# Kernel optimization log

Measured on AMD Instinct MI355X. Metric: run time of the kernel, lower is better.

## Reference

```python
import jax, jax.numpy as jnp
import numpy as np

B, N_LATENT, N_NUISANCE, N_OUT = 2048, 64, 16, 2048


def setup_inputs() -> dict:
    key = jax.random.key(0)
    ks = jax.random.split(key, 6)
    z = jax.random.normal(ks[0], (B, N_LATENT + N_NUISANCE), dtype=jnp.float32)
    size_factor = jax.random.uniform(ks[1], (B, 1), dtype=jnp.float32) + 0.5
    # nn.Linear(n_latent, n_out, bias=False): store as [L, O] for z0 @ W
    amat_w = jax.random.normal(ks[2], (N_LATENT, N_OUT), dtype=jnp.float32) / np.sqrt(N_LATENT).astype(np.float32)
    amat_site = jax.random.normal(ks[3], (N_NUISANCE, N_LATENT, N_OUT), dtype=jnp.float32)
    offsets = jax.random.normal(ks[4], (N_NUISANCE, N_OUT), dtype=jnp.float32)
    px_r = jax.random.normal(ks[5], (N_OUT,), dtype=jnp.float32)
    return {"z": z, "size_factor": size_factor, "amat_w": amat_w,
            "amat_site": amat_site, "offsets": offsets, "px_r": px_r}


def reference(z, size_factor, amat_w, amat_site, offsets, px_r):
    n_nuisance = offsets.shape[0]
    nuisance_oh = z[..., -n_nuisance:]          # [B, N] one-hot site indicator
    z0 = z[..., :-n_nuisance]                   # [B, L] latent part
    x1 = z0 @ amat_w                            # [B, O] shared linear decoder
    nuisance_ids = jnp.argmax(nuisance_oh, axis=-1)  # [B] int ids
    # dropout(p=0.1) in eval mode == identity; .detach() -> stop_gradient
    z0_d = jax.lax.stop_gradient(z0)
    As = amat_site[nuisance_ids]                # [B, L, O] per-sample gathered weights
    x2 = jnp.einsum('bl,blo->bo', z0_d, As)     # batched matvec reduction over L
    mu = jax.nn.softmax(x1 + x2 + offsets[nuisance_ids], axis=-1)  # [B, O]
    mu = mu * size_factor                       # scale by per-cell size factor
    theta = jnp.exp(px_r)                       # NB inverse-dispersion, [O]
    return mu, theta
```

## Files before the change

### kernel.cpp

```cpp
#include <hip/hip_runtime.h>
#include <hip/hip_bf16.h>

#define NB 2048
#define NL 64
#define NN 16
#define NROW 80
#define NO 2048
#define TPB 256
#define OPT 8
#define G 4
#define MAXWL (NB / G + NN)
#define MBLK (NN * NL * NO / 4 / TPB)

typedef unsigned int   u32;
typedef unsigned short u16;

__device__ __forceinline__ float bflo(u32 u) { union { u32 i; float f; } c; c.i = u << 16;          return c.f; }
__device__ __forceinline__ float bfhi(u32 u) { union { u32 i; float f; } c; c.i = u & 0xffff0000u;  return c.f; }
__device__ __forceinline__ u16 f2bf(float f) { __hip_bfloat16 h = __float2bfloat16(f); return *(u16*)&h; }

__global__ __launch_bounds__(TPB) void prep(
    const float* __restrict__ W,
    const float* __restrict__ A,
    const float* __restrict__ z,
    const float* __restrict__ pxr,
    u16* __restrict__ M,
    u32* __restrict__ counts,
    u32* __restrict__ perm,
    u32* __restrict__ wl,
    u32* __restrict__ nit,
    float* __restrict__ out)
{
    const int blk = blockIdx.x;
    const int tid = threadIdx.x;

    if (blk < MBLK) {
        size_t t    = (size_t)blk * TPB + tid;
        size_t base = t * 4;
        float4 w = *(const float4*)(W + (base & (size_t)(NL * NO - 1)));
        float4 a = *(const float4*)(A + base);
        ushort4 m;
        m.x = f2bf(w.x + a.x);
        m.y = f2bf(w.y + a.y);
        m.z = f2bf(w.z + a.z);
        m.w = f2bf(w.w + a.w);
        *(ushort4*)(M + base) = m;
        return;
    }

    if (blk == MBLK) {
        __shared__ u32 lc[NN];
        __shared__ u32 choff[NN + 1];
        if (tid < NN) lc[tid] = 0;
        __syncthreads();
        #pragma unroll
        for (int k = 0; k < NB / TPB; ++k) {
            const int b = k * TPB + tid;
            const float* zp = z + (size_t)b * NROW + NL;
            float4 v0 = *(const float4*)(zp);
            float4 v1 = *(const float4*)(zp + 4);
            float4 v2 = *(const float4*)(zp + 8);
            float4 v3 = *(const float4*)(zp + 12);
            float best = v0.x; int bi = 0;
            #define CK(val, idx) if ((val) > best) { best = (val); bi = (idx); }
            CK(v0.y, 1)  CK(v0.z, 2)  CK(v0.w, 3)
            CK(v1.x, 4)  CK(v1.y, 5)  CK(v1.z, 6)  CK(v1.w, 7)
            CK(v2.x, 8)  CK(v2.y, 9)  CK(v2.z, 10) CK(v2.w, 11)
            CK(v3.x, 12) CK(v3.y, 13) CK(v3.z, 14) CK(v3.w, 15)
            #undef CK
            u32 pos = atomicAdd(&lc[bi], 1u);
            perm[(u32)bi * NB + pos] = (u32)b;
        }
        __syncthreads();
        if (tid == 0) {
            u32 n = 0;
            for (int i = 0; i < NN; ++i) { choff[i] = n; n += (lc[i] + G - 1) / G; }
            choff[NN] = n;
            nit[0] = n;
        }
        __syncthreads();
        if (tid < NN) {
            counts[tid] = lc[tid];
            const u32 nch = (lc[tid] + G - 1) / G;
            const u32 off = choff[tid];
            for (u32 c = 0; c < nch; ++c) wl[off + c] = ((u32)tid << 16) | c;
        }
        return;
    }

    for (int o = tid; o < NO; o += TPB)
        out[(size_t)NB * NO + o] = __expf(pxr[o]);
}

__global__ __launch_bounds__(TPB) void decoder_g(
    const float* __restrict__ z,
    const float* __restrict__ sf,
    const u16*   __restrict__ M,
    const float* __restrict__ offs,
    const u32*   __restrict__ counts,
    const u32*   __restrict__ perm,
    const u32*   __restrict__ wl,
    const u32*   __restrict__ nit,
    float* __restrict__ out)
{
    if (blockIdx.x >= nit[0]) return;
    const u32 w      = wl[blockIdx.x];
    const int bucket = (int)(w >> 16);
    const int chunk  = (int)(w & 0xffffu);
    const u32 cnt    = counts[bucket];
    const int tid    = threadIdx.x;

    __shared__ float zt[NL][G];
    __shared__ float s_sf[G];
    __shared__ u32   s_rows[G];
    __shared__ float s_red[2][G][4];

    if (tid < G) {
        u32 idx = (u32)(chunk * G + tid);
        u32 clamped = idx < cnt ? idx : (cnt - 1u);
        u32 r = perm[(size_t)bucket * NB + clamped];
        s_rows[tid] = r;
        s_sf[tid]   = sf[r];
    }
    __syncthreads();
    {
        const int l = tid & (NL - 1);
        const int g = tid >> 6;
        zt[l][g] = z[(size_t)s_rows[g] * NROW + l];
    }
    __syncthreads();

    const int o0 = tid * OPT;
    const uint4* mv = (const uint4*)(M + (size_t)bucket * (NL * NO) + o0);

    float acc[G][OPT];
    {
        float4 oa = *(const float4*)(offs + bucket * NO + o0);
        float4 ob = *(const float4*)(offs + bucket * NO + o0 + 4);
        #pragma unroll
        for (int g = 0; g < G; ++g) {
            acc[g][0] = oa.x; acc[g][1] = oa.y; acc[g][2] = oa.z; acc[g][3] = oa.w;
            acc[g][4] = ob.x; acc[g][5] = ob.y; acc[g][6] = ob.z; acc[g][7] = ob.w;
        }
    }

    #pragma unroll 8
    for (int l = 0; l < NL; ++l) {
        const uint4 m = mv[l * (NO / OPT)];
        float v[OPT];
        v[0] = bflo(m.x); v[1] = bfhi(m.x);
        v[2] = bflo(m.y); v[3] = bfhi(m.y);
        v[4] = bflo(m.z); v[5] = bfhi(m.z);
        v[6] = bflo(m.w); v[7] = bfhi(m.w);
        const float4 za = *(const float4*)(&zt[l][0]);
        const float zg[G] = { za.x, za.y, za.z, za.w };
        #pragma unroll
        for (int g = 0; g < G; ++g)
            #pragma unroll
            for (int j = 0; j < OPT; ++j)
                acc[g][j] += zg[g] * v[j];
    }

    const int wv = tid >> 6;
    #pragma unroll
    for (int g = 0; g < G; ++g) {
        float m = acc[g][0];
        #pragma unroll
        for (int j = 1; j < OPT; ++j) m = fmaxf(m, acc[g][j]);
        #pragma unroll
        for (int off = 32; off > 0; off >>= 1) m = fmaxf(m, __shfl_down(m, off));
        if ((tid & 63) == 0) s_red[0][g][wv] = m;
    }
    __syncthreads();
    float mx[G];
    #pragma unroll
    for (int g = 0; g < G; ++g)
        mx[g] = fmaxf(fmaxf(s_red[0][g][0], s_red[0][g][1]),
                      fmaxf(s_red[0][g][2], s_red[0][g][3]));

    #pragma unroll
    for (int g = 0; g < G; ++g) {
        float s = 0.f;
        #pragma unroll
        for (int j = 0; j < OPT; ++j) { acc[g][j] = __expf(acc[g][j] - mx[g]); s += acc[g][j]; }
        #pragma unroll
        for (int off = 32; off > 0; off >>= 1) s += __shfl_down(s, off);
        if ((tid & 63) == 0) s_red[1][g][wv] = s;
    }
    __syncthreads();
    #pragma unroll
    for (int g = 0; g < G; ++g) {
        if ((u32)(chunk * G + g) < cnt) {
            const float sm  = (s_red[1][g][0] + s_red[1][g][1]) + (s_red[1][g][2] + s_red[1][g][3]);
            const float scl = s_sf[g] / sm;
            float* op = out + (size_t)s_rows[g] * NO + o0;
            *(float4*)(op)     = make_float4(acc[g][0] * scl, acc[g][1] * scl, acc[g][2] * scl, acc[g][3] * scl);
            *(float4*)(op + 4) = make_float4(acc[g][4] * scl, acc[g][5] * scl, acc[g][6] * scl, acc[g][7] * scl);
        }
    }
}

__global__ __launch_bounds__(TPB) void decoder_f(
    const float* __restrict__ z, const float* __restrict__ sf,
    const float* __restrict__ W, const float* __restrict__ A,
    const float* __restrict__ offs, const float* __restrict__ pxr,
    float* __restrict__ out)
{
    const int b   = blockIdx.x;
    const int tid = threadIdx.x;
    if (b == NB) {
        for (int o = tid; o < NO; o += TPB)
            out[(size_t)NB * NO + o] = __expf(pxr[o]);
        return;
    }
    __shared__ float z0s[NL];
    __shared__ int   s_id;
    __shared__ float s_red[6];
    if (tid < NL) z0s[tid] = z[b * NROW + tid];
    if (tid == 0) {
        float best = -1e30f; int bi = 0;
        for (int i = 0; i < NN; ++i) {
            float v = z[b * NROW + NL + i];
            if (v > best) { best = v; bi = i; }
        }
        s_id = bi;
    }
    __syncthreads();
    const int id = s_id;
    const int o0 = tid * OPT;
    const float* wp = W + o0;
    const float* ap = A + (size_t)id * NL * NO + o0;
    float acc[OPT];
    {
        float4 oa = *(const float4*)(offs + id * NO + o0);
        float4 ob = *(const float4*)(offs + id * NO + o0 + 4);
        acc[0] = oa.x; acc[1] = oa.y; acc[2] = oa.z; acc[3] = oa.w;
        acc[4] = ob.x; acc[5] = ob.y; acc[6] = ob.z; acc[7] = ob.w;
    }
    #pragma unroll 4
    for (int l = 0; l < NL; ++l) {
        const float zl = z0s[l];
        float4 w0 = *(const float4*)(wp + l * NO);
        float4 w1 = *(const float4*)(wp + l * NO + 4);
        float4 a0 = *(const float4*)(ap + l * NO);
        float4 a1 = *(const float4*)(ap + l * NO + 4);
        acc[0] += zl * (w0.x + a0.x); acc[1] += zl * (w0.y + a0.y);
        acc[2] += zl * (w0.z + a0.z); acc[3] += zl * (w0.w + a0.w);
        acc[4] += zl * (w1.x + a1.x); acc[5] += zl * (w1.y + a1.y);
        acc[6] += zl * (w1.z + a1.z); acc[7] += zl * (w1.w + a1.w);
    }
    float m = acc[0];
    #pragma unroll
    for (int j = 1; j < OPT; ++j) m = fmaxf(m, acc[j]);
    #pragma unroll
    for (int off = 32; off > 0; off >>= 1) m = fmaxf(m, __shfl_down(m, off));
    if ((tid & 63) == 0) s_red[tid >> 6] = m;
    __syncthreads();
    if (tid == 0) s_red[4] = fmaxf(fmaxf(s_red[0], s_red[1]), fmaxf(s_red[2], s_red[3]));
    __syncthreads();
    const float mx = s_red[4];
    float ex[OPT];
    float s = 0.f;
    #pragma unroll
    for (int j = 0; j < OPT; ++j) { ex[j] = __expf(acc[j] - mx); s += ex[j]; }
    #pragma unroll
    for (int off = 32; off > 0; off >>= 1) s += __shfl_down(s, off);
    if ((tid & 63) == 0) s_red[tid >> 6] = s;
    __syncthreads();
    if (tid == 0) s_red[5] = (s_red[0] + s_red[1]) + (s_red[2] + s_red[3]);
    __syncthreads();
    const float scale = sf[b] / s_red[5];
    float* op = out + (size_t)b * NO + o0;
    *(float4*)(op)     = make_float4(ex[0] * scale, ex[1] * scale, ex[2] * scale, ex[3] * scale);
    *(float4*)(op + 4) = make_float4(ex[4] * scale, ex[5] * scale, ex[6] * scale, ex[7] * scale);
}

extern "C" void kernel_launch(void* const* d_in, const int* in_sizes, int n_in,
                              void* d_out, int out_size, void* d_ws, size_t ws_size,
                              hipStream_t stream) {
    const float* z    = (const float*)d_in[0];
    const float* sf   = (const float*)d_in[1];
    const float* W    = (const float*)d_in[2];
    const float* A    = (const float*)d_in[3];
    const float* offs = (const float*)d_in[4];
    const float* pxr  = (const float*)d_in[5];
    float* out = (float*)d_out;

    const size_t m_bytes = (size_t)NN * NL * NO * sizeof(u16);
    const size_t p_bytes = (size_t)NN * NB * sizeof(u32);
    const size_t need    = m_bytes + 256 + p_bytes + (MAXWL + 64) * sizeof(u32);
    if (ws_size >= need) {
        u16* M      = (u16*)d_ws;
        u32* counts = (u32*)((char*)d_ws + m_bytes);
        u32* perm   = (u32*)((char*)d_ws + m_bytes + 256);
        u32* wl     = (u32*)((char*)d_ws + m_bytes + 256 + p_bytes);
        u32* nit    = wl + MAXWL;
        hipLaunchKernelGGL(prep, dim3(MBLK + 2), dim3(TPB), 0, stream,
                           W, A, z, pxr, M, counts, perm, wl, nit, out);
        hipLaunchKernelGGL(decoder_g, dim3(MAXWL), dim3(TPB), 0, stream,
                           z, sf, M, offs, counts, perm, wl, nit, out);
    } else {
        hipLaunchKernelGGL(decoder_f, dim3(NB + 1), dim3(TPB), 0, stream,
                           z, sf, W, A, offs, pxr, out);
    }
}
```

Baseline: 107.6 us.

## Use bf16 MFMA with transposed weight layout and 16-row groups in decoder

Replaces the scalar FMA decoder with an MFMA 16x16x32 bf16 kernel that processes 16 same-site rows per 512-thread block. The prep step now writes the merged site weights transposed to [bucket][O][L] so each lane can load contiguous k-slices as MFMA operands. z is split into bf16 high and low parts to recover near-fp32 accuracy, at the cost of twice the MFMA work. Larger groups mean each weight tile is reused across more rows, but padded tail rows in small buckets waste more work.

```diff
diff --git a/kernel.cpp b/kernel.cpp
--- a/kernel.cpp
+++ b/kernel.cpp
@@ -7,24 +7,30 @@
 #define NROW 80
 #define NO 2048
 #define TPB 256
+#define TPB_D 512
+#define G 16
+#define MAXWL (NB / G + NN)
+#define PBLK 256
 #define OPT 8
-#define G 4
-#define MAXWL (NB / G + NN)
-#define MBLK (NN * NL * NO / 4 / TPB)
 
 typedef unsigned int   u32;
 typedef unsigned short u16;
+typedef __attribute__((ext_vector_type(8))) short short8;
+typedef __attribute__((ext_vector_type(4))) float f32x4;
 
 __device__ __forceinline__ float bflo(u32 u) { union { u32 i; float f; } c; c.i = u << 16;          return c.f; }
-__device__ __forceinline__ float bfhi(u32 u) { union { u32 i; float f; } c; c.i = u & 0xffff0000u;  return c.f; }
 __device__ __forceinline__ u16 f2bf(float f) { __hip_bfloat16 h = __float2bfloat16(f); return *(u16*)&h; }
+
+__device__ __forceinline__ f32x4 mfma16(short8 a, short8 b, f32x4 c) {
+    return __builtin_amdgcn_mfma_f32_16x16x32_bf16(a, b, c, 0, 0, 0);
+}
 
 __global__ __launch_bounds__(TPB) void prep(
     const float* __restrict__ W,
     const float* __restrict__ A,
     const float* __restrict__ z,
     const float* __restrict__ pxr,
-    u16* __restrict__ M,
+    u16* __restrict__ Mt,
     u32* __restrict__ counts,
     u32* __restrict__ perm,
     u32* __restrict__ wl,
@@ -34,21 +40,29 @@
     const int blk = blockIdx.x;
     const int tid = threadIdx.x;
 
-    if (blk < MBLK) {
-        size_t t    = (size_t)blk * TPB + tid;
-        size_t base = t * 4;
-        float4 w = *(const float4*)(W + (base & (size_t)(NL * NO - 1)));
-        float4 a = *(const float4*)(A + base);
-        ushort4 m;
-        m.x = f2bf(w.x + a.x);
-        m.y = f2bf(w.y + a.y);
-        m.z = f2bf(w.z + a.z);
-        m.w = f2bf(w.w + a.w);
-        *(ushort4*)(M + base) = m;
+    if (blk < PBLK) {
+        const int bucket = blk >> 4;
+        const int rem    = blk & 15;
+        const int och    = rem >> 1;
+        const int k0     = (rem & 1) * 32;
+        const int o      = (och << 8) | tid;
+        const float* wp = W + (size_t)k0 * NO + o;
+        const float* ap = A + (size_t)bucket * NL * NO + (size_t)k0 * NO + o;
+        u32 pk[16];
+        #pragma unroll
+        for (int j = 0; j < 16; ++j) {
+            float v0 = wp[(2 * j) * NO]     + ap[(2 * j) * NO];
+            float v1 = wp[(2 * j + 1) * NO] + ap[(2 * j + 1) * NO];
+            pk[j] = (u32)f2bf(v0) | ((u32)f2bf(v1) << 16);
+        }
+        u16* row = Mt + ((size_t)bucket * NO + o) * NL + k0;
+        #pragma unroll
+        for (int i = 0; i < 4; ++i)
+            *(uint4*)(row + i * 8) = make_uint4(pk[4 * i], pk[4 * i + 1], pk[4 * i + 2], pk[4 * i + 3]);
         return;
     }
 
-    if (blk == MBLK) {
+    if (blk == PBLK) {
         __shared__ u32 lc[NN];
         __shared__ u32 choff[NN + 1];
         if (tid < NN) lc[tid] = 0;
@@ -75,7 +89,6 @@
         if (tid == 0) {
             u32 n = 0;
             for (int i = 0; i < NN; ++i) { choff[i] = n; n += (lc[i] + G - 1) / G; }
-            choff[NN] = n;
             nit[0] = n;
         }
         __syncthreads();
@@ -92,10 +105,10 @@
         out[(size_t)NB * NO + o] = __expf(pxr[o]);
 }
 
-__global__ __launch_bounds__(TPB) void decoder_g(
+__global__ __launch_bounds__(TPB_D) void decoder_t(
     const float* __restrict__ z,
     const float* __restrict__ sf,
-    const u16*   __restrict__ M,
+    const u16*   __restrict__ Mt,
     const float* __restrict__ offs,
     const u32*   __restrict__ counts,
     const u32*   __restrict__ perm,
@@ -108,94 +121,105 @@
     const int bucket = (int)(w >> 16);
     const int chunk  = (int)(w & 0xffffu);
     const u32 cnt    = counts[bucket];
-    const int tid    = threadIdx.x;
-
-    __shared__ float zt[NL][G];
+    const int tid  = threadIdx.x;
+    const int lane = tid & 63;
+    const int wv   = tid >> 6;
+    const int r    = lane & 15;
+    const int q    = lane >> 4;
+
+    __shared__ u32   s_rows[G];
     __shared__ float s_sf[G];
-    __shared__ u32   s_rows[G];
-    __shared__ float s_red[2][G][4];
+    __shared__ float red[2][G][8];
 
     if (tid < G) {
         u32 idx = (u32)(chunk * G + tid);
-        u32 clamped = idx < cnt ? idx : (cnt - 1u);
-        u32 r = perm[(size_t)bucket * NB + clamped];
-        s_rows[tid] = r;
-        s_sf[tid]   = sf[r];
-    }
-    __syncthreads();
+        u32 cl  = idx < cnt ? idx : cnt - 1u;
+        u32 rr  = perm[(size_t)bucket * NB + cl];
+        s_rows[tid] = rr;
+        s_sf[tid]   = sf[rr];
+    }
+    __syncthreads();
+
+    union BF { short8 s; u32 u[4]; };
+    BF bh[2], bl[2];
     {
-        const int l = tid & (NL - 1);
-        const int g = tid >> 6;
-        zt[l][g] = z[(size_t)s_rows[g] * NROW + l];
-    }
-    __syncthreads();
-
-    const int o0 = tid * OPT;
-    const uint4* mv = (const uint4*)(M + (size_t)bucket * (NL * NO) + o0);
-
-    float acc[G][OPT];
-    {
-        float4 oa = *(const float4*)(offs + bucket * NO + o0);
-        float4 ob = *(const float4*)(offs + bucket * NO + o0 + 4);
-        #pragma unroll
-        for (int g = 0; g < G; ++g) {
-            acc[g][0] = oa.x; acc[g][1] = oa.y; acc[g][2] = oa.z; acc[g][3] = oa.w;
-            acc[g][4] = ob.x; acc[g][5] = ob.y; acc[g][6] = ob.z; acc[g][7] = ob.w;
-        }
-    }
-
-    #pragma unroll 8
-    for (int l = 0; l < NL; ++l) {
-        const uint4 m = mv[l * (NO / OPT)];
-        float v[OPT];
-        v[0] = bflo(m.x); v[1] = bfhi(m.x);
-        v[2] = bflo(m.y); v[3] = bfhi(m.y);
-        v[4] = bflo(m.z); v[5] = bfhi(m.z);
-        v[6] = bflo(m.w); v[7] = bfhi(m.w);
-        const float4 za = *(const float4*)(&zt[l][0]);
-        const float zg[G] = { za.x, za.y, za.z, za.w };
-        #pragma unroll
-        for (int g = 0; g < G; ++g)
+        const float* zp = z + (size_t)s_rows[r] * NROW + (q << 3);
+        #pragma unroll
+        for (int kk = 0; kk < 2; ++kk) {
+            float4 za = *(const float4*)(zp + kk * 32);
+            float4 zb = *(const float4*)(zp + kk * 32 + 4);
+            float e[8] = { za.x, za.y, za.z, za.w, zb.x, zb.y, zb.z, zb.w };
             #pragma unroll
-            for (int j = 0; j < OPT; ++j)
-                acc[g][j] += zg[g] * v[j];
-    }
-
-    const int wv = tid >> 6;
-    #pragma unroll
-    for (int g = 0; g < G; ++g) {
-        float m = acc[g][0];
-        #pragma unroll
-        for (int j = 1; j < OPT; ++j) m = fmaxf(m, acc[g][j]);
-        #pragma unroll
-        for (int off = 32; off > 0; off >>= 1) m = fmaxf(m, __shfl_down(m, off));
-        if ((tid & 63) == 0) s_red[0][g][wv] = m;
-    }
-    __syncthreads();
-    float mx[G];
-    #pragma unroll
-    for (int g = 0; g < G; ++g)
-        mx[g] = fmaxf(fmaxf(s_red[0][g][0], s_red[0][g][1]),
-                      fmaxf(s_red[0][g][2], s_red[0][g][3]));
-
-    #pragma unroll
-    for (int g = 0; g < G; ++g) {
-        float s = 0.f;
-        #pragma unroll
-        for (int j = 0; j < OPT; ++j) { acc[g][j] = __expf(acc[g][j] - mx[g]); s += acc[g][j]; }
-        #pragma unroll
-        for (int off = 32; off > 0; off >>= 1) s += __shfl_down(s, off);
-        if ((tid & 63) == 0) s_red[1][g][wv] = s;
-    }
-    __syncthreads();
-    #pragma unroll
-    for (int g = 0; g < G; ++g) {
-        if ((u32)(chunk * G + g) < cnt) {
-            const float sm  = (s_red[1][g][0] + s_red[1][g][1]) + (s_red[1][g][2] + s_red[1][g][3]);
-            const float scl = s_sf[g] / sm;
-            float* op = out + (size_t)s_rows[g] * NO + o0;
-            *(float4*)(op)     = make_float4(acc[g][0] * scl, acc[g][1] * scl, acc[g][2] * scl, acc[g][3] * scl);
-            *(float4*)(op + 4) = make_float4(acc[g][4] * scl, acc[g][5] * scl, acc[g][6] * scl, acc[g][7] * scl);
+            for (int j = 0; j < 4; ++j) {
+                u16 h0 = f2bf(e[2 * j]);
+                u16 h1 = f2bf(e[2 * j + 1]);
+                float l0 = e[2 * j]     - bflo(h0);
+                float l1 = e[2 * j + 1] - bflo(h1);
+                bh[kk].u[j] = (u32)h0 | ((u32)h1 << 16);
+                bl[kk].u[j] = (u32)f2bf(l0) | ((u32)f2bf(l1) << 16);
+            }
+        }
+    }
+
+    f32x4 acc[16];
+    const u16*   mtb = Mt   + (size_t)bucket * NO * NL;
+    const float* ofb = offs + (size_t)bucket * NO;
+    #pragma unroll
+    for (int t = 0; t < 16; ++t) {
+        const int tg = (wv << 4) + t;
+        const u16* ar = mtb + ((size_t)((tg << 4) + r)) * NL + (q << 3);
+        uint4 a0r = *(const uint4*)(ar);
+        uint4 a1r = *(const uint4*)(ar + 32);
+        short8 a0, a1;
+        __builtin_memcpy(&a0, &a0r, 16);
+        __builtin_memcpy(&a1, &a1r, 16);
+        float4 of = *(const float4*)(ofb + (tg << 4) + (q << 2));
+        f32x4 c = { of.x, of.y, of.z, of.w };
+        c = mfma16(a0, bh[0].s, c);
+        c = mfma16(a1, bh[1].s, c);
+        c = mfma16(a0, bl[0].s, c);
+        c = mfma16(a1, bl[1].s, c);
+        acc[t] = c;
+    }
+
+    float mx = acc[0][0];
+    #pragma unroll
+    for (int t = 0; t < 16; ++t)
+        #pragma unroll
+        for (int j = 0; j < 4; ++j) mx = fmaxf(mx, acc[t][j]);
+    mx = fmaxf(mx, __shfl_xor(mx, 16));
+    mx = fmaxf(mx, __shfl_xor(mx, 32));
+    if (lane < G) red[0][lane][wv] = mx;
+    __syncthreads();
+    float m = red[0][r][0];
+    #pragma unroll
+    for (int i = 1; i < 8; ++i) m = fmaxf(m, red[0][r][i]);
+
+    float s = 0.f;
+    #pragma unroll
+    for (int t = 0; t < 16; ++t)
+        #pragma unroll
+        for (int j = 0; j < 4; ++j) {
+            float e = __expf(acc[t][j] - m);
+            acc[t][j] = e;
+            s += e;
+        }
+    s += __shfl_xor(s, 16);
+    s += __shfl_xor(s, 32);
+    if (lane < G) red[1][lane][wv] = s;
+    __syncthreads();
+    float tot = red[1][r][0];
+    #pragma unroll
+    for (int i = 1; i < 8; ++i) tot += red[1][r][i];
+
+    if ((u32)(chunk * G + r) < cnt) {
+        const float scl = s_sf[r] / tot;
+        float* ob = out + (size_t)s_rows[r] * NO;
+        #pragma unroll
+        for (int t = 0; t < 16; ++t) {
+            const int tg = (wv << 4) + t;
+            *(float4*)(ob + (tg << 4) + (q << 2)) =
+                make_float4(acc[t][0] * scl, acc[t][1] * scl, acc[t][2] * scl, acc[t][3] * scl);
         }
     }
 }
@@ -290,15 +314,15 @@
     const size_t p_bytes = (size_t)NN * NB * sizeof(u32);
     const size_t need    = m_bytes + 256 + p_bytes + (MAXWL + 64) * sizeof(u32);
     if (ws_size >= need) {
-        u16* M      = (u16*)d_ws;
+        u16* Mt     = (u16*)d_ws;
         u32* counts = (u32*)((char*)d_ws + m_bytes);
         u32* perm   = (u32*)((char*)d_ws + m_bytes + 256);
         u32* wl     = (u32*)((char*)d_ws + m_bytes + 256 + p_bytes);
         u32* nit    = wl + MAXWL;
-        hipLaunchKernelGGL(prep, dim3(MBLK + 2), dim3(TPB), 0, stream,
-                           W, A, z, pxr, M, counts, perm, wl, nit, out);
-        hipLaunchKernelGGL(decoder_g, dim3(MAXWL), dim3(TPB), 0, stream,
-                           z, sf, M, offs, counts, perm, wl, nit, out);
+        hipLaunchKernelGGL(prep, dim3(PBLK + 2), dim3(TPB), 0, stream,
+                           W, A, z, pxr, Mt, counts, perm, wl, nit, out);
+        hipLaunchKernelGGL(decoder_t, dim3(MAXWL), dim3(TPB_D), 0, stream,
+                           z, sf, Mt, offs, counts, perm, wl, nit, out);
     } else {
         hipLaunchKernelGGL(decoder_f, dim3(NB + 1), dim3(TPB), 0, stream,
                            z, sf, W, A, offs, pxr, out);
```

New measurement: 100.4 us. -6.7%, faster.
